# Performance work log

Measured on AMD Instinct MI355X. Metric: run time of the kernel, lower is better.

Reference implementation:

```python
import jax, jax.numpy as jnp
import numpy as np

N = 8192
IN_F = 512
OUT_F = 512
N_SUB = 8


def setup_inputs() -> dict:
    key = jax.random.key(0)
    k1, k2, k3, k4 = jax.random.split(key, 4)
    input_features = jax.random.normal(k1, (N, IN_F), dtype=jnp.float32)
    # dense adjacency with small positive entries (normalized-adj-like)
    adj = jax.random.uniform(k2, (N, N), dtype=jnp.float32) / N
    subspace_labels = jax.random.randint(k3, (N,), 0, N_SUB, dtype=jnp.int32)
    # kaiming-uniform-style init per subspace weight
    bound = float(np.sqrt(6.0 / IN_F))
    W = jax.random.uniform(k4, (N_SUB, IN_F, OUT_F), dtype=jnp.float32,
                           minval=-bound, maxval=bound)
    return {"input_features": input_features, "adj": adj,
            "subspace_labels": subspace_labels, "W": W}


def reference(input_features, adj, subspace_labels, W):
    # Original: for each subspace s,
    #   output[mask_s] = adj[mask_s][:, mask_s] @ (X[mask_s] @ W[s])
    # Equivalently: per-node support uses that node's subspace weight, and
    # adjacency is masked to same-subspace pairs.
    n_sub = W.shape[0]
    support = jnp.zeros((input_features.shape[0], W.shape[2]),
                        dtype=input_features.dtype)
    for s in range(n_sub):  # small fixed loop over subspaces
        sel = (subspace_labels == s)[:, None]
        support = support + jnp.where(sel, input_features @ W[s], 0.0)
    # mask adjacency to intra-subspace edges: [N, N]
    same = (subspace_labels[:, None] == subspace_labels[None, :])
    masked_adj = jnp.where(same, adj, 0.0)
    return masked_adj @ support
```

## Files before the change

### kernel.cpp

```cpp
#include <hip/hip_runtime.h>
#include <hip/hip_bf16.h>

#define NN   8192
#define FF   512
#define NS   8
#define CAP  1152
#define KKT  (NS * CAP)

typedef __bf16 bf16x8 __attribute__((ext_vector_type(8)));
typedef float  f32x4  __attribute__((ext_vector_type(4)));

__global__ void bucket_kernel(const int* __restrict__ labels,
                              int* __restrict__ permP,
                              int* __restrict__ kk_of) {
    __shared__ int off8[NS];
    int t = threadIdx.x;
    if (t < NS) off8[t] = 0;
    for (int i = t; i < KKT; i += 256) permP[i] = -1;
    __syncthreads();
    for (int i = t; i < NN; i += 256) {
        int s = labels[i];
        int p = atomicAdd(&off8[s], 1);
        if (p < CAP) {
            int pos = s * CAP + p;
            permP[pos] = i;
            kk_of[i] = pos;
        } else {
            kk_of[i] = -1;
        }
    }
}

__global__ void wt_kernel(const float* __restrict__ W, __bf16* __restrict__ WT) {
    __shared__ float tile[32][33];
    int s  = blockIdx.z;
    int n0 = blockIdx.x * 32, k0 = blockIdx.y * 32;
    int tx = threadIdx.x, ty = threadIdx.y;
    const float* Ws = W + (size_t)s * FF * FF;
    for (int r = 0; r < 4; ++r) {
        int k = k0 + ty + r * 8;
        tile[ty + r * 8][tx] = Ws[(size_t)k * FF + n0 + tx];
    }
    __syncthreads();
    __bf16* WTs = WT + (size_t)s * FF * FF;
    for (int r = 0; r < 4; ++r) {
        int n = n0 + ty + r * 8;
        WTs[(size_t)n * FF + k0 + tx] = (__bf16)tile[tx][ty + r * 8];
    }
}

__global__ __launch_bounds__(512) void support_kernel(
        const float* __restrict__ X, const __bf16* __restrict__ WT,
        const int* __restrict__ permP, __bf16* __restrict__ supT) {
    __shared__ __align__(16) __bf16 Alds[4][32][8];
    __shared__ __align__(16) __bf16 Blds[4][512][8];
    __shared__ int nodes[32];
    const int t = threadIdx.x, lane = t & 63, w = t >> 6;
    const int ii0 = blockIdx.x * 32;
    const int seg = ii0 / CAP;
    const int mh = w & 1, nq = w >> 1, l15 = lane & 15, q = lane >> 4;
    f32x4 acc[8] = {};
    if (t < 32) nodes[t] = permP[ii0 + t];
    __syncthreads();
    const __bf16* Wseg = WT + (size_t)seg * FF * FF;
    for (int k0 = 0; k0 < FF; k0 += 32) {
        #pragma unroll
        for (int pass = 0; pass < 4; ++pass) {
            int slot = pass * 512 + t;
            int c = slot & 3, n = slot >> 2;
            uint4 tmp = *(const uint4*)(Wseg + (size_t)n * FF + k0 + c * 8);
            *(uint4*)&Blds[c][n][0] = tmp;
        }
        if (t < 256) {
            int m = t >> 3, c = t & 7;
            int node = nodes[m];
            __align__(8) __bf16 v[4];
            if (node >= 0) {
                float4 xv = *(const float4*)(X + (size_t)node * FF + k0 + c * 4);
                v[0] = (__bf16)xv.x; v[1] = (__bf16)xv.y;
                v[2] = (__bf16)xv.z; v[3] = (__bf16)xv.w;
            } else {
                v[0] = v[1] = v[2] = v[3] = (__bf16)0.0f;
            }
            int kq = c >> 1, off = (c & 1) * 4;
            *(uint2*)&Alds[kq][m][off] = *(uint2*)v;
        }
        __syncthreads();
        bf16x8 af = *(bf16x8*)&Alds[q][mh * 16 + l15][0];
        int nbase = nq * 128 + l15;
        #pragma unroll
        for (int nt = 0; nt < 8; ++nt) {
            bf16x8 bfr = *(bf16x8*)&Blds[q][nbase + nt * 16][0];
            acc[nt] = __builtin_amdgcn_mfma_f32_16x16x32_bf16(af, bfr, acc[nt], 0, 0, 0);
        }
        __syncthreads();
    }
    int kkb = ii0 + mh * 16 + q * 4;
    #pragma unroll
    for (int nt = 0; nt < 8; ++nt) {
        int n = nq * 128 + nt * 16 + l15;
        __align__(8) __bf16 v[4];
        #pragma unroll
        for (int r = 0; r < 4; ++r) v[r] = (__bf16)acc[nt][r];
        *(uint2*)(supT + (size_t)n * KKT + kkb) = *(uint2*)v;
    }
}

__global__ __launch_bounds__(256) void compact_kernel(
        const float* __restrict__ adj, const int* __restrict__ permP,
        const int* __restrict__ kk_of, __bf16* __restrict__ adjc) {
    int ii = blockIdx.x;
    int node = permP[ii];
    if (node < 0) return;
    int base = (ii / CAP) * CAP;
    __bf16* dst = adjc + (size_t)ii * CAP;
    const float4* arow = (const float4*)(adj + (size_t)node * NN);
    const int4*  kkrow = (const int4*)kk_of;
    int t = threadIdx.x;
    #pragma unroll
    for (int p = 0; p < NN / (256 * 4); ++p) {
        int idx = p * 256 + t;
        float4 a = arow[idx];
        int4  kk = kkrow[idx];
        int j;
        j = kk.x - base; if ((unsigned)j < CAP) dst[j] = (__bf16)a.x;
        j = kk.y - base; if ((unsigned)j < CAP) dst[j] = (__bf16)a.y;
        j = kk.z - base; if ((unsigned)j < CAP) dst[j] = (__bf16)a.z;
        j = kk.w - base; if ((unsigned)j < CAP) dst[j] = (__bf16)a.w;
    }
}

__global__ __launch_bounds__(512) void gemm_kernel(
        const __bf16* __restrict__ adjc, const __bf16* __restrict__ supT,
        const int* __restrict__ permP, float* __restrict__ out) {
    __shared__ __align__(16) __bf16 Alds[4][32][8];
    __shared__ __align__(16) __bf16 Blds[4][512][8];
    const int t = threadIdx.x, lane = t & 63, w = t >> 6;
    const int ii0 = blockIdx.x * 32;
    const int seg = ii0 / CAP, base = seg * CAP;
    const int mh = w & 1, nq = w >> 1, l15 = lane & 15, q = lane >> 4;
    f32x4 acc[8] = {};
    const __bf16* Ag = adjc + (size_t)ii0 * CAP;
    for (int j0 = 0; j0 < CAP; j0 += 32) {
        #pragma unroll
        for (int pass = 0; pass < 4; ++pass) {
            int slot = pass * 512 + t;
            int c = slot & 3, n = slot >> 2;
            uint4 tmp = *(const uint4*)(supT + (size_t)n * KKT + base + j0 + c * 8);
            *(uint4*)&Blds[c][n][0] = tmp;
        }
        if (t < 128) {
            int m = t >> 2, c = t & 3;
            uint4 tmp = *(const uint4*)(Ag + (size_t)m * CAP + j0 + c * 8);
            *(uint4*)&Alds[c][m][0] = tmp;
        }
        __syncthreads();
        bf16x8 af = *(bf16x8*)&Alds[q][mh * 16 + l15][0];
        int nbase = nq * 128 + l15;
        #pragma unroll
        for (int nt = 0; nt < 8; ++nt) {
            bf16x8 bfr = *(bf16x8*)&Blds[q][nbase + nt * 16][0];
            acc[nt] = __builtin_amdgcn_mfma_f32_16x16x32_bf16(af, bfr, acc[nt], 0, 0, 0);
        }
        __syncthreads();
    }
    int rowb = ii0 + mh * 16 + q * 4;
    #pragma unroll
    for (int r = 0; r < 4; ++r) {
        int node = permP[rowb + r];
        if (node >= 0) {
            float* o = out + (size_t)node * FF + nq * 128 + l15;
            #pragma unroll
            for (int nt = 0; nt < 8; ++nt) o[nt * 16] = acc[nt][r];
        }
    }
}

extern "C" void kernel_launch(void* const* d_in, const int* in_sizes, int n_in,
                              void* d_out, int out_size, void* d_ws, size_t ws_size,
                              hipStream_t stream) {
    const float* X      = (const float*)d_in[0];
    const float* adj    = (const float*)d_in[1];
    const int*   labels = (const int*)d_in[2];
    const float* W      = (const float*)d_in[3];
    float* out = (float*)d_out;

    char* ws = (char*)d_ws;
    int*    kk_of = (int*)(ws + 1024);
    int*    permP = (int*)(ws + (64u << 10));
    __bf16* WT    = (__bf16*)(ws + (1u << 20));
    __bf16* supT  = (__bf16*)(ws + (6u << 20));
    __bf16* adjc  = (__bf16*)(ws + (16u << 20));

    hipMemsetAsync(adjc, 0, (size_t)KKT * CAP * sizeof(__bf16), stream);
    bucket_kernel<<<1, 256, 0, stream>>>(labels, permP, kk_of);
    wt_kernel<<<dim3(16, 16, 8), dim3(32, 8), 0, stream>>>(W, WT);
    support_kernel<<<KKT / 32, 512, 0, stream>>>(X, WT, permP, supT);
    compact_kernel<<<KKT, 256, 0, stream>>>(adj, permP, kk_of, adjc);
    gemm_kernel<<<KKT / 32, 512, 0, stream>>>(adjc, supT, permP, out);
}
```

Before: 513.7 us.

## Fuse prep kernels, compact adjacency rows in LDS, split GEMMs over output columns

Merges the W transpose and label bucketing into one prep kernel, with the bucketing now using wave-aggregated ballot atomics. The compact kernel builds four rows per block in LDS, zero-filled there, and writes them out contiguously, which drops the separate memset of the compacted adjacency and its scattered bf16 global stores. The support and GEMM kernels drop to 256 threads and split the 512 output columns over a second grid dimension, doubling block count, and pad their LDS arrays. These aim to cut launch overhead and memset traffic and to raise occupancy, at the cost of re-reading A tiles once per column half.

Result: slower. 529.9 us (+3.2%).

```diff
diff --git a/kernel.cpp b/kernel.cpp
--- a/kernel.cpp
+++ b/kernel.cpp
@@ -10,80 +10,91 @@
 typedef __bf16 bf16x8 __attribute__((ext_vector_type(8)));
 typedef float  f32x4  __attribute__((ext_vector_type(4)));
 
-__global__ void bucket_kernel(const int* __restrict__ labels,
-                              int* __restrict__ permP,
-                              int* __restrict__ kk_of) {
-    __shared__ int off8[NS];
-    int t = threadIdx.x;
-    if (t < NS) off8[t] = 0;
-    for (int i = t; i < KKT; i += 256) permP[i] = -1;
-    __syncthreads();
-    for (int i = t; i < NN; i += 256) {
-        int s = labels[i];
-        int p = atomicAdd(&off8[s], 1);
-        if (p < CAP) {
-            int pos = s * CAP + p;
-            permP[pos] = i;
-            kk_of[i] = pos;
-        } else {
-            kk_of[i] = -1;
-        }
-    }
-}
-
-__global__ void wt_kernel(const float* __restrict__ W, __bf16* __restrict__ WT) {
-    __shared__ float tile[32][33];
-    int s  = blockIdx.z;
-    int n0 = blockIdx.x * 32, k0 = blockIdx.y * 32;
-    int tx = threadIdx.x, ty = threadIdx.y;
-    const float* Ws = W + (size_t)s * FF * FF;
-    for (int r = 0; r < 4; ++r) {
-        int k = k0 + ty + r * 8;
-        tile[ty + r * 8][tx] = Ws[(size_t)k * FF + n0 + tx];
-    }
-    __syncthreads();
-    __bf16* WTs = WT + (size_t)s * FF * FF;
-    for (int r = 0; r < 4; ++r) {
-        int n = n0 + ty + r * 8;
-        WTs[(size_t)n * FF + k0 + tx] = (__bf16)tile[tx][ty + r * 8];
-    }
-}
-
-__global__ __launch_bounds__(512) void support_kernel(
+__global__ __launch_bounds__(256) void prep_kernel(
+        const float* __restrict__ W, __bf16* __restrict__ WT,
+        const int* __restrict__ labels, int* __restrict__ permP,
+        int* __restrict__ kk_of) {
+    if (blockIdx.x < 2048) {
+        __shared__ float tile[32][33];
+        const int id = blockIdx.x;
+        const int n0 = (id & 15) * 32, k0 = ((id >> 4) & 15) * 32, s = id >> 8;
+        const int t = threadIdx.x, tx = t & 31, ty = t >> 5;
+        const float* Ws = W + (size_t)s * FF * FF;
+        #pragma unroll
+        for (int r = 0; r < 4; ++r)
+            tile[ty + r * 8][tx] = Ws[(size_t)(k0 + ty + r * 8) * FF + n0 + tx];
+        __syncthreads();
+        __bf16* WTs = WT + (size_t)s * FF * FF;
+        #pragma unroll
+        for (int r = 0; r < 4; ++r)
+            WTs[(size_t)(n0 + ty + r * 8) * FF + k0 + tx] = (__bf16)tile[tx][ty + r * 8];
+    } else {
+        __shared__ int off8[NS];
+        const int t = threadIdx.x, lane = t & 63;
+        if (t < NS) off8[t] = 0;
+        for (int i = t; i < KKT; i += 256) permP[i] = -1;
+        __syncthreads();
+        for (int i = t; i < NN; i += 256) {
+            int s = labels[i];
+            int pos = -1;
+            #pragma unroll
+            for (int ss = 0; ss < NS; ++ss) {
+                unsigned long long mask = __ballot(s == ss);
+                if (s == ss) {
+                    int leader = __ffsll((unsigned long long)mask) - 1;
+                    int nbelow = __popcll(mask & ((1ull << lane) - 1ull));
+                    int base = 0;
+                    if (lane == leader) base = atomicAdd(&off8[ss], __popcll(mask));
+                    base = __shfl(base, leader);
+                    pos = base + nbelow;
+                }
+            }
+            if (pos >= 0 && pos < CAP) {
+                int kk = s * CAP + pos;
+                permP[kk] = i;
+                kk_of[i] = kk;
+            } else {
+                kk_of[i] = -1;
+            }
+        }
+    }
+}
+
+__global__ __launch_bounds__(256) void support_kernel(
         const float* __restrict__ X, const __bf16* __restrict__ WT,
         const int* __restrict__ permP, __bf16* __restrict__ supT) {
-    __shared__ __align__(16) __bf16 Alds[4][32][8];
-    __shared__ __align__(16) __bf16 Blds[4][512][8];
+    __shared__ __align__(16) __bf16 Alds[4][33][8];
+    __shared__ __align__(16) __bf16 Blds[4][257][8];
     __shared__ int nodes[32];
     const int t = threadIdx.x, lane = t & 63, w = t >> 6;
     const int ii0 = blockIdx.x * 32;
+    const int ncol0 = blockIdx.y * 256;
     const int seg = ii0 / CAP;
     const int mh = w & 1, nq = w >> 1, l15 = lane & 15, q = lane >> 4;
     f32x4 acc[8] = {};
     if (t < 32) nodes[t] = permP[ii0 + t];
     __syncthreads();
     const __bf16* Wseg = WT + (size_t)seg * FF * FF;
+    const int am = t >> 3, ac = t & 7;
     for (int k0 = 0; k0 < FF; k0 += 32) {
         #pragma unroll
         for (int pass = 0; pass < 4; ++pass) {
-            int slot = pass * 512 + t;
-            int c = slot & 3, n = slot >> 2;
-            uint4 tmp = *(const uint4*)(Wseg + (size_t)n * FF + k0 + c * 8);
-            *(uint4*)&Blds[c][n][0] = tmp;
-        }
-        if (t < 256) {
-            int m = t >> 3, c = t & 7;
-            int node = nodes[m];
+            int slot = pass * 256 + t;
+            int cc = slot & 3, n = slot >> 2;
+            *(uint4*)&Blds[cc][n][0] =
+                *(const uint4*)(Wseg + (size_t)(ncol0 + n) * FF + k0 + cc * 8);
+        }
+        {
+            int node = nodes[am];
             __align__(8) __bf16 v[4];
             if (node >= 0) {
-                float4 xv = *(const float4*)(X + (size_t)node * FF + k0 + c * 4);
+                float4 xv = *(const float4*)(X + (size_t)node * FF + k0 + ac * 4);
                 v[0] = (__bf16)xv.x; v[1] = (__bf16)xv.y;
                 v[2] = (__bf16)xv.z; v[3] = (__bf16)xv.w;
             } else {
                 v[0] = v[1] = v[2] = v[3] = (__bf16)0.0f;
             }
-            int kq = c >> 1, off = (c & 1) * 4;
-            *(uint2*)&Alds[kq][m][off] = *(uint2*)v;
+            *(uint2*)&Alds[ac >> 1][am][(ac & 1) * 4] = *(uint2*)v;
         }
         __syncthreads();
         bf16x8 af = *(bf16x8*)&Alds[q][mh * 16 + l15][0];
@@ -98,7 +109,7 @@
     int kkb = ii0 + mh * 16 + q * 4;
     #pragma unroll
     for (int nt = 0; nt < 8; ++nt) {
-        int n = nq * 128 + nt * 16 + l15;
+        int n = ncol0 + nq * 128 + nt * 16 + l15;
         __align__(8) __bf16 v[4];
         #pragma unroll
         for (int r = 0; r < 4; ++r) v[r] = (__bf16)acc[nt][r];
@@ -109,34 +120,46 @@
 __global__ __launch_bounds__(256) void compact_kernel(
         const float* __restrict__ adj, const int* __restrict__ permP,
         const int* __restrict__ kk_of, __bf16* __restrict__ adjc) {
-    int ii = blockIdx.x;
-    int node = permP[ii];
-    if (node < 0) return;
-    int base = (ii / CAP) * CAP;
-    __bf16* dst = adjc + (size_t)ii * CAP;
-    const float4* arow = (const float4*)(adj + (size_t)node * NN);
-    const int4*  kkrow = (const int4*)kk_of;
-    int t = threadIdx.x;
+    __shared__ __align__(16) __bf16 rows[4][CAP];
+    const int t = threadIdx.x;
+    const int ii0 = blockIdx.x * 4;
+    const int base = (ii0 / CAP) * CAP;
+    for (int j = t; j < 4 * CAP / 2; j += 256) ((unsigned int*)rows)[j] = 0u;
+    int nodes[4];
+    #pragma unroll
+    for (int r = 0; r < 4; ++r) nodes[r] = permP[ii0 + r];
+    __syncthreads();
+    const int4* kkrow = (const int4*)kk_of;
     #pragma unroll
     for (int p = 0; p < NN / (256 * 4); ++p) {
         int idx = p * 256 + t;
-        float4 a = arow[idx];
-        int4  kk = kkrow[idx];
-        int j;
-        j = kk.x - base; if ((unsigned)j < CAP) dst[j] = (__bf16)a.x;
-        j = kk.y - base; if ((unsigned)j < CAP) dst[j] = (__bf16)a.y;
-        j = kk.z - base; if ((unsigned)j < CAP) dst[j] = (__bf16)a.z;
-        j = kk.w - base; if ((unsigned)j < CAP) dst[j] = (__bf16)a.w;
-    }
-}
-
-__global__ __launch_bounds__(512) void gemm_kernel(
+        int4 kk = kkrow[idx];
+        kk.x -= base; kk.y -= base; kk.z -= base; kk.w -= base;
+        #pragma unroll
+        for (int r = 0; r < 4; ++r) {
+            int node = nodes[r];
+            if (node < 0) continue;
+            float4 a = *(const float4*)(adj + (size_t)node * NN + (size_t)idx * 4);
+            if ((unsigned)kk.x < CAP) rows[r][kk.x] = (__bf16)a.x;
+            if ((unsigned)kk.y < CAP) rows[r][kk.y] = (__bf16)a.y;
+            if ((unsigned)kk.z < CAP) rows[r][kk.z] = (__bf16)a.z;
+            if ((unsigned)kk.w < CAP) rows[r][kk.w] = (__bf16)a.w;
+        }
+    }
+    __syncthreads();
+    const uint4* src = (const uint4*)rows;
+    uint4* dst = (uint4*)(adjc + (size_t)ii0 * CAP);
+    for (int j = t; j < 4 * CAP * 2 / 16; j += 256) dst[j] = src[j];
+}
+
+__global__ __launch_bounds__(256) void gemm_kernel(
         const __bf16* __restrict__ adjc, const __bf16* __restrict__ supT,
         const int* __restrict__ permP, float* __restrict__ out) {
-    __shared__ __align__(16) __bf16 Alds[4][32][8];
-    __shared__ __align__(16) __bf16 Blds[4][512][8];
+    __shared__ __align__(16) __bf16 Alds[4][33][8];
+    __shared__ __align__(16) __bf16 Blds[4][257][8];
     const int t = threadIdx.x, lane = t & 63, w = t >> 6;
     const int ii0 = blockIdx.x * 32;
+    const int ncol0 = blockIdx.y * 256;
     const int seg = ii0 / CAP, base = seg * CAP;
     const int mh = w & 1, nq = w >> 1, l15 = lane & 15, q = lane >> 4;
     f32x4 acc[8] = {};
@@ -144,15 +167,15 @@
     for (int j0 = 0; j0 < CAP; j0 += 32) {
         #pragma unroll
         for (int pass = 0; pass < 4; ++pass) {
-            int slot = pass * 512 + t;
-            int c = slot & 3, n = slot >> 2;
-            uint4 tmp = *(const uint4*)(supT + (size_t)n * KKT + base + j0 + c * 8);
-            *(uint4*)&Blds[c][n][0] = tmp;
+            int slot = pass * 256 + t;
+            int cc = slot & 3, n = slot >> 2;
+            *(uint4*)&Blds[cc][n][0] =
+                *(const uint4*)(supT + (size_t)(ncol0 + n) * KKT + base + j0 + cc * 8);
         }
         if (t < 128) {
-            int m = t >> 2, c = t & 3;
-            uint4 tmp = *(const uint4*)(Ag + (size_t)m * CAP + j0 + c * 8);
-            *(uint4*)&Alds[c][m][0] = tmp;
+            int m = t >> 2, cc = t & 3;
+            *(uint4*)&Alds[cc][m][0] =
+                *(const uint4*)(Ag + (size_t)m * CAP + j0 + cc * 8);
         }
         __syncthreads();
         bf16x8 af = *(bf16x8*)&Alds[q][mh * 16 + l15][0];
@@ -169,7 +192,7 @@
     for (int r = 0; r < 4; ++r) {
         int node = permP[rowb + r];
         if (node >= 0) {
-            float* o = out + (size_t)node * FF + nq * 128 + l15;
+            float* o = out + (size_t)node * FF + ncol0 + nq * 128 + l15;
             #pragma unroll
             for (int nt = 0; nt < 8; ++nt) o[nt * 16] = acc[nt][r];
         }
@@ -192,10 +215,8 @@
     __bf16* supT  = (__bf16*)(ws + (6u << 20));
     __bf16* adjc  = (__bf16*)(ws + (16u << 20));
 
-    hipMemsetAsync(adjc, 0, (size_t)KKT * CAP * sizeof(__bf16), stream);
-    bucket_kernel<<<1, 256, 0, stream>>>(labels, permP, kk_of);
-    wt_kernel<<<dim3(16, 16, 8), dim3(32, 8), 0, stream>>>(W, WT);
-    support_kernel<<<KKT / 32, 512, 0, stream>>>(X, WT, permP, supT);
-    compact_kernel<<<KKT, 256, 0, stream>>>(adj, permP, kk_of, adjc);
-    gemm_kernel<<<KKT / 32, 512, 0, stream>>>(adjc, supT, permP, out);
-}
+    prep_kernel<<<2049, 256, 0, stream>>>(W, WT, labels, permP, kk_of);
+    support_kernel<<<dim3(KKT / 32, 2), 256, 0, stream>>>(X, WT, permP, supT);
+    compact_kernel<<<KKT / 4, 256, 0, stream>>>(adj, permP, kk_of, adjc);
+    gemm_kernel<<<dim3(KKT / 32, 2), 256, 0, stream>>>(adjc, supT, permP, out);
+}
```
